# Kernel tuning notes

Measured on AMD Instinct MI355X. Metric: run time of the kernel, lower is better.

## Reference

```python
import jax, jax.numpy as jnp
import numpy as np

D_MODEL = 1024
NUM_HEADS = 16
BATCH = 2
SEQ = 2048


def setup_inputs() -> dict:
    key = jax.random.key(0)
    ks = jax.random.split(key, 5)
    scale = 1.0 / np.sqrt(D_MODEL)
    x = jax.random.normal(ks[0], (BATCH, SEQ, D_MODEL), dtype=jnp.float32)
    Wq = jax.random.normal(ks[1], (D_MODEL, D_MODEL), dtype=jnp.float32) * scale
    Wk = jax.random.normal(ks[2], (D_MODEL, D_MODEL), dtype=jnp.float32) * scale
    Wv = jax.random.normal(ks[3], (D_MODEL, D_MODEL), dtype=jnp.float32) * scale
    Wo = jax.random.normal(ks[4], (D_MODEL, D_MODEL), dtype=jnp.float32) * scale
    return {"x": x, "Wq": Wq, "Wk": Wk, "Wv": Wv, "Wo": Wo}


def reference(x, Wq, Wk, Wv, Wo):
    b, s, d_model = x.shape
    h = NUM_HEADS
    d_head = d_model // h
    # projections (Linear with weight [out,in]: y = x @ W^T)
    def split_heads(y):
        return y.reshape(b, s, h, d_head).transpose(0, 2, 1, 3)  # b h s d
    q = split_heads(x @ Wq.T)
    k = split_heads(x @ Wk.T)
    v = split_heads(x @ Wv.T)
    # full (non-flash) attention, as in the original
    att = jnp.einsum('bhsd,bhtd->bhst', q, k) / jnp.sqrt(jnp.float32(d_head)).astype(x.dtype)
    att = jax.nn.softmax(att, axis=-1)
    out = jnp.einsum('bhst,bhtd->bhsd', att, v)
    out = out.transpose(0, 2, 1, 3).reshape(b, s, d_model)
    return out @ Wo.T
```

## Files before the change

kernel.cpp:

```cpp
#include <hip/hip_runtime.h>
#include <stdint.h>

typedef __bf16 bf16_t;
typedef __bf16 bf16x4 __attribute__((ext_vector_type(4)));
typedef __bf16 bf16x8 __attribute__((ext_vector_type(8)));
typedef float  f32x4  __attribute__((ext_vector_type(4)));
typedef float  f32x16 __attribute__((ext_vector_type(16)));

#define D_MODEL 1024
#define SEQ     2048
#define BATCH   2
#define NHEAD   16
#define DHEAD   64
#define NROWS   (BATCH*SEQ)
#define LDT     72

#define QSCALE  (0.125f * 1.4426950408889634f)

__device__ __forceinline__ void async_ld16(const bf16_t* g, bf16_t* l) {
    __builtin_amdgcn_global_load_lds(
        (const __attribute__((address_space(1))) uint32_t*)(uintptr_t)g,
        (__attribute__((address_space(3))) uint32_t*)(uintptr_t)l,
        16, 0, 0);
}

__device__ __forceinline__ bf16x8 cvt8(f32x4 lo, f32x4 hi) {
    bf16x8 o;
#pragma unroll
    for (int i = 0; i < 4; ++i) { o[i] = (bf16_t)lo[i]; o[4 + i] = (bf16_t)hi[i]; }
    return o;
}

__device__ __forceinline__ void plswap(uint32_t& a, uint32_t& b) {
    asm("v_permlane32_swap_b32 %0, %1" : "+v"(a), "+v"(b));
}

__device__ __forceinline__ uint32_t cvtpk(float lo, float hi) {
    uint32_t r;
    asm("v_cvt_pk_bf16_f32 %0, %1, %2" : "=v"(r) : "v"(lo), "v"(hi));
    return r;
}

__global__ void __launch_bounds__(256)
k_cvt(const float* __restrict__ w0, const float* __restrict__ w1,
      const float* __restrict__ w2, const float* __restrict__ w3,
      const float* __restrict__ x,
      bf16_t* __restrict__ o0, bf16_t* __restrict__ o1,
      bf16_t* __restrict__ o2, bf16_t* __restrict__ o3,
      bf16_t* __restrict__ ox)
{
    const int blk = blockIdx.x;
    const float* s; bf16_t* d; int bi;
    if (blk < 2048) { s = x; d = ox; bi = blk; }
    else {
        const int t = blk - 2048, sel = t >> 9; bi = t & 511;
        s = (sel == 0) ? w0 : (sel == 1) ? w1 : (sel == 2) ? w2 : w3;
        d = (sel == 0) ? o0 : (sel == 1) ? o1 : (sel == 2) ? o2 : o3;
    }
    const size_t i = ((size_t)bi * 256 + threadIdx.x) * 8;
    *(bf16x8*)(d + i) = cvt8(*(const f32x4*)(s + i), *(const f32x4*)(s + i + 4));
}

template <int OUT_MODE, int MT>
__device__ __forceinline__ void gemmT(bf16_t* __restrict__ smem,
                                      const bf16_t* __restrict__ X,
                                      const bf16_t* __restrict__ W,
                                      void* __restrict__ Yv,
                                      int m0, int n0, float oscale)
{
    constexpr int FM = MT / 32;
    bf16_t* lA = smem;
    bf16_t* lB = smem + MT * 32;

    const int tid  = threadIdx.x;
    const int lane = tid & 63;
    const int w    = tid >> 6;
    const int l15  = lane & 15;
    const int quad = lane >> 4;

    const int cB0 = tid, cB1 = tid + 256;
    const int rB0 = cB0 >> 2, rB1 = cB1 >> 2;
    const int kB0 = (cB0 & 3) ^ ((rB0 >> 1) & 3);
    const int kB1 = (cB1 & 3) ^ ((rB1 >> 1) & 3);
    const bf16_t* gB0 = W + (size_t)(n0 + rB0) * D_MODEL + kB0 * 8;
    const bf16_t* gB1 = W + (size_t)(n0 + rB1) * D_MODEL + kB1 * 8;

    const int cA0 = tid;
    const int rA0 = cA0 >> 2;
    const int kA0 = (cA0 & 3) ^ ((rA0 >> 1) & 3);
    const bf16_t* gA0 = X + (size_t)(m0 + rA0) * D_MODEL + kA0 * 8;
    const int cA1 = tid + 256;
    const int rA1 = cA1 >> 2;
    const int kA1 = (cA1 & 3) ^ ((rA1 >> 1) & 3);
    const bf16_t* gA1 = X + (size_t)(m0 + rA1) * D_MODEL + kA1 * 8;

    int am[FM], bn[4];
    const int mw = (w >> 1) * (MT / 2), nw = (w & 1) * 64;
#pragma unroll
    for (int i = 0; i < FM; ++i) {
        const int ra = mw + i * 16 + l15;
        am[i] = ra * 32 + (quad ^ ((ra >> 1) & 3)) * 8;
    }
#pragma unroll
    for (int i = 0; i < 4; ++i) {
        const int rb = nw + i * 16 + l15;
        bn[i] = rb * 32 + (quad ^ ((rb >> 1) & 3)) * 8;
    }

    f32x4 acc[FM][4];
#pragma unroll
    for (int i = 0; i < FM; ++i)
#pragma unroll
        for (int j = 0; j < 4; ++j) acc[i][j] = f32x4{0.f, 0.f, 0.f, 0.f};

    for (int k0 = 0; k0 < D_MODEL; k0 += 32) {
        __syncthreads();
        async_ld16(gA0 + k0, &lA[cA0 * 8]);
        if constexpr (MT == 128) async_ld16(gA1 + k0, &lA[cA1 * 8]);
        async_ld16(gB0 + k0, &lB[cB0 * 8]);
        async_ld16(gB1 + k0, &lB[cB1 * 8]);
        __syncthreads();

        bf16x8 af[FM], bfr[4];
#pragma unroll
        for (int i = 0; i < FM; ++i) af[i] = *(const bf16x8*)&lA[am[i]];
#pragma unroll
        for (int i = 0; i < 4; ++i) bfr[i] = *(const bf16x8*)&lB[bn[i]];
#pragma unroll
        for (int mi = 0; mi < FM; ++mi)
#pragma unroll
            for (int ni = 0; ni < 4; ++ni)
                acc[mi][ni] = __builtin_amdgcn_mfma_f32_16x16x32_bf16(
                    af[mi], bfr[ni], acc[mi][ni], 0, 0, 0);
    }

    if constexpr (OUT_MODE == 1) {
        bf16_t* lT = smem;
#pragma unroll
        for (int h0 = 0; h0 < 2; ++h0) {
            __syncthreads();
            if ((w >> 1) == h0) {
#pragma unroll
                for (int mi = 0; mi < FM; ++mi)
#pragma unroll
                    for (int ni = 0; ni < 4; ++ni) {
                        bf16x4 pk;
#pragma unroll
                        for (int r = 0; r < 4; ++r)
                            pk[r] = (bf16_t)(acc[mi][ni][r] * oscale);
                        const int col = nw + ni * 16 + l15;
                        *(bf16x4*)&lT[col * LDT + mi * 16 + quad * 4] = pk;
                    }
            }
            __syncthreads();
            const int col = tid & 127;
            const int seg = tid >> 7;
            const int brow = m0 + h0 * 64;
            const int b = brow >> 11, sb = brow & 2047;
            const int cg = n0 + col;
            bf16_t* dst = (bf16_t*)Yv +
                ((size_t)((b << 4) | (cg >> 6)) * 64 + (cg & 63)) * SEQ + sb;
#pragma unroll
            for (int u = 0; u < 4; ++u)
                *(bf16x8*)(dst + seg * 32 + u * 8) =
                    *(const bf16x8*)&lT[col * LDT + seg * 32 + u * 8];
        }
    } else {
#pragma unroll
        for (int mi = 0; mi < FM; ++mi)
#pragma unroll
            for (int ni = 0; ni < 4; ++ni)
#pragma unroll
                for (int r = 0; r < 4; ++r) {
                    const int row = m0 + mw + mi * 16 + quad * 4 + r;
                    const int col = n0 + nw + ni * 16 + l15;
                    const float vv = acc[mi][ni][r] * oscale;
                    if constexpr (OUT_MODE == 0)
                        ((bf16_t*)Yv)[(size_t)row * D_MODEL + col] = (bf16_t)vv;
                    else
                        ((float*)Yv)[(size_t)row * D_MODEL + col] = vv;
                }
    }
}

__global__ void __launch_bounds__(256, 3)
k_gemm_qkv(const bf16_t* __restrict__ X,
           const bf16_t* __restrict__ Wq, const bf16_t* __restrict__ Wk,
           const bf16_t* __restrict__ Wv,
           bf16_t* __restrict__ Qb, bf16_t* __restrict__ Kb, bf16_t* __restrict__ Vt)
{
    __shared__ __align__(16) bf16_t smem[128 * LDT];
    const int id = blockIdx.x + 32 * blockIdx.y;
    const int s  = (id & 7) * 96 + (id >> 3);
    const int m0 = (s & 31) * 128;
    const int yp = s >> 5;
    const int sel = yp >> 3;
    const int n0  = (yp & 7) * 128;
    if (sel == 0)      gemmT<0,128>(smem, X, Wq, Qb, m0, n0, QSCALE);
    else if (sel == 1) gemmT<0,128>(smem, X, Wk, Kb, m0, n0, 1.0f);
    else               gemmT<1,128>(smem, X, Wv, Vt, m0, n0, 1.0f);
}

__global__ void __launch_bounds__(256, 2)
k_gemm_out(const bf16_t* __restrict__ X, const bf16_t* __restrict__ W,
           float* __restrict__ Y)
{
    __shared__ __align__(16) bf16_t smem[64 * 32 + 128 * 32];
    const int id = blockIdx.x + 64 * blockIdx.y;
    const int s  = (id & 7) * 64 + (id >> 3);
    const int m0 = (s & 63) * 64;
    const int n0 = (s >> 6) * 128;
    gemmT<2,64>(smem, X, W, Y, m0, n0, 1.0f);
}

__global__ void __launch_bounds__(256, 2)
k_attn(const bf16_t* __restrict__ Qb, const bf16_t* __restrict__ Kb,
       const bf16_t* __restrict__ Vt, bf16_t* __restrict__ Ob)
{
    __shared__ __align__(16) char arena[51200];
    bf16_t* lK = (bf16_t*)arena;
    bf16_t* lV = (bf16_t*)(arena + 24576);

    const int tid  = threadIdx.x;
    const int lane = tid & 63;
    const int w    = tid >> 6;
    const int wq   = w >> 1;
    const int wk   = w & 1;
    const int l31  = lane & 31;
    const int h    = lane >> 5;

    const int i_  = blockIdx.x + 32 * blockIdx.y;
    const int bh  = 4 * (i_ & 7) + ((i_ >> 3) & 3);
    const int q0  = (i_ >> 5) * 128;
    const int b_ = bh >> 4, hh = bh & 15;

    const size_t base = (size_t)b_ * SEQ * D_MODEL + (size_t)hh * DHEAD;
    const bf16_t* Qp = Qb + base;
    const bf16_t* Kp = Kb + base;
    const bf16_t* Vp = Vt + (size_t)bh * DHEAD * SEQ;

    bf16x8 qf[2][4];
#pragma unroll
    for (int qh = 0; qh < 2; ++qh) {
        const int qrow = q0 + wq * 64 + qh * 32 + l31;
#pragma unroll
        for (int c = 0; c < 4; ++c)
            qf[qh][c] = *(const bf16x8*)&Qp[(size_t)qrow * D_MODEL + c * 16 + h * 8];
    }

    const int c0 = tid, c1 = tid + 256;
    const int r0 = c0 >> 3, g0 = (c0 & 7) ^ (r0 & 7);
    const int r1 = r0 + 32;
    const bf16_t* gK0 = Kp + (size_t)r0 * D_MODEL + g0 * 8;
    const bf16_t* gK1 = Kp + (size_t)r1 * D_MODEL + g0 * 8;
    const bf16_t* gV0 = Vp + (size_t)r0 * SEQ + g0 * 8;
    const bf16_t* gV1 = Vp + (size_t)r1 * SEQ + g0 * 8;

    int koff[4], voff[2][2];
#pragma unroll
    for (int c = 0; c < 4; ++c) {
        const int row = wk * 32 + l31;
        koff[c] = row * 64 + (((2 * c + h) ^ (row & 7)) * 8);
    }
#pragma unroll
    for (int a = 0; a < 2; ++a)
#pragma unroll
        for (int ck = 0; ck < 2; ++ck) {
            const int row = a * 32 + l31;
            const int ch  = 4 * wk + 2 * ck + h;
            voff[a][ck] = row * 64 + ((ch ^ (row & 7)) * 8);
        }

    bf16x8 onef;
#pragma unroll
    for (int i = 0; i < 8; ++i) onef[i] = (bf16_t)1.0f;

    f32x16 fz;
#pragma unroll
    for (int i = 0; i < 16; ++i) fz[i] = 0.f;

    f32x16 acc_o[2][2];
    f32x16 acc_s[2];
#pragma unroll
    for (int qh = 0; qh < 2; ++qh) {
#pragma unroll
        for (int i = 0; i < 16; ++i) {
            acc_o[qh][0][i] = 0.f; acc_o[qh][1][i] = 0.f; acc_s[qh][i] = 0.f;
        }
    }

    auto STAGE = [&](int tile, int buf) {
        const size_t kv0 = (size_t)tile * 64;
        bf16_t* dK = lK + buf * 4096;
        bf16_t* dV = lV + buf * 4096;
        async_ld16(gK0 + kv0 * D_MODEL, &dK[c0 * 8]);
        async_ld16(gK1 + kv0 * D_MODEL, &dK[c1 * 8]);
        async_ld16(gV0 + kv0, &dV[c0 * 8]);
        async_ld16(gV1 + kv0, &dV[c1 * 8]);
    };

    STAGE(0, 0);
    STAGE(1, 1);
    asm volatile("s_waitcnt vmcnt(4)\n\ts_barrier" ::: "memory");

    int cb = 0;
    const int NT = SEQ / 64;
    for (int t = 0; t < NT; ++t) {
        if (t + 2 < NT) STAGE(t + 2, cb == 0 ? 2 : cb - 1);
        const bf16_t* lKc = lK + cb * 4096;
        const bf16_t* lVc = lV + cb * 4096;

        bf16x8 kf[4];
#pragma unroll
        for (int c = 0; c < 4; ++c) kf[c] = *(const bf16x8*)&lKc[koff[c]];

        f32x16 st[2];
        __builtin_amdgcn_s_setprio(1);
#pragma unroll
        for (int qh = 0; qh < 2; ++qh) {
            st[qh] = __builtin_amdgcn_mfma_f32_32x32x16_bf16(
                kf[0], qf[qh][0], fz, 0, 0, 0);
#pragma unroll
            for (int c = 1; c < 4; ++c)
                st[qh] = __builtin_amdgcn_mfma_f32_32x32x16_bf16(
                    kf[c], qf[qh][c], st[qh], 0, 0, 0);
        }
        __builtin_amdgcn_s_setprio(0);

        uint32_t pd[2][4][2];
#pragma unroll
        for (int qh = 0; qh < 2; ++qh)
#pragma unroll
            for (int g = 0; g < 4; ++g) {
                pd[qh][g][0] = cvtpk(__builtin_amdgcn_exp2f(st[qh][g * 4 + 0]),
                                     __builtin_amdgcn_exp2f(st[qh][g * 4 + 1]));
                pd[qh][g][1] = cvtpk(__builtin_amdgcn_exp2f(st[qh][g * 4 + 2]),
                                     __builtin_amdgcn_exp2f(st[qh][g * 4 + 3]));
            }

        bf16x8 pf[2][2];
#pragma unroll
        for (int qh = 0; qh < 2; ++qh)
#pragma unroll
            for (int ck = 0; ck < 2; ++ck) {
                uint32_t a0 = pd[qh][2 * ck][0],     b0 = pd[qh][2 * ck + 1][0];
                uint32_t a1 = pd[qh][2 * ck][1],     b1 = pd[qh][2 * ck + 1][1];
                plswap(a0, b0);
                plswap(a1, b1);
                union { bf16x8 v; uint32_t d[4]; } up;
                up.d[0] = a0; up.d[1] = a1; up.d[2] = b0; up.d[3] = b1;
                pf[qh][ck] = up.v;
            }

        __builtin_amdgcn_s_setprio(1);
#pragma unroll
        for (int qh = 0; qh < 2; ++qh)
#pragma unroll
            for (int ck = 0; ck < 2; ++ck)
                acc_s[qh] = __builtin_amdgcn_mfma_f32_32x32x16_bf16(
                    pf[qh][ck], onef, acc_s[qh], 0, 0, 0);
#pragma unroll
        for (int a = 0; a < 2; ++a)
#pragma unroll
            for (int ck = 0; ck < 2; ++ck) {
                bf16x8 vf = *(const bf16x8*)&lVc[voff[a][ck]];
#pragma unroll
                for (int qh = 0; qh < 2; ++qh)
                    acc_o[qh][a] = __builtin_amdgcn_mfma_f32_32x32x16_bf16(
                        pf[qh][ck], vf, acc_o[qh][a], 0, 0, 0);
            }
        __builtin_amdgcn_s_setprio(0);

        if (t + 2 < NT)
            asm volatile("s_waitcnt vmcnt(4) lgkmcnt(0)\n\ts_barrier" ::: "memory");
        else
            asm volatile("s_waitcnt vmcnt(0) lgkmcnt(0)\n\ts_barrier" ::: "memory");
        cb = (cb == 2) ? 0 : cb + 1;
    }

    union F16 { f32x16 v; f32x4 q[4]; };
    float* blob = (float*)arena + ((size_t)(wq * 64 + lane)) * 100;

    if (wk) {
#pragma unroll
        for (int qh = 0; qh < 2; ++qh) {
#pragma unroll
            for (int a = 0; a < 2; ++a) {
                F16 u; u.v = acc_o[qh][a];
#pragma unroll
                for (int i = 0; i < 4; ++i)
                    *(f32x4*)&blob[(qh * 8 + a * 4 + i) * 4] = u.q[i];
            }
            F16 s; s.v = acc_s[qh];
#pragma unroll
            for (int i = 0; i < 4; ++i)
                *(f32x4*)&blob[64 + (qh * 4 + i) * 4] = s.q[i];
        }
    }
    __syncthreads();
    if (!wk) {
#pragma unroll
        for (int qh = 0; qh < 2; ++qh) {
#pragma unroll
            for (int a = 0; a < 2; ++a) {
                F16 u; u.v = acc_o[qh][a];
#pragma unroll
                for (int i = 0; i < 4; ++i)
                    u.q[i] += *(const f32x4*)&blob[(qh * 8 + a * 4 + i) * 4];
                acc_o[qh][a] = u.v;
            }
            F16 s; s.v = acc_s[qh];
#pragma unroll
            for (int i = 0; i < 4; ++i)
                s.q[i] += *(const f32x4*)&blob[64 + (qh * 4 + i) * 4];
            acc_s[qh] = s.v;
        }

#pragma unroll
        for (int qh = 0; qh < 2; ++qh)
#pragma unroll
            for (int g = 0; g < 4; ++g)
#pragma unroll
                for (int r = 0; r < 4; ++r) {
                    const float inv = 1.0f / acc_s[qh][g * 4 + r];
                    const int row = b_ * SEQ + q0 + wq * 64 + qh * 32 + (r + 8 * g + 4 * h);
                    const size_t rb = (size_t)row * D_MODEL + hh * DHEAD + l31;
                    Ob[rb]      = (bf16_t)(acc_o[qh][0][g * 4 + r] * inv);
                    Ob[rb + 32] = (bf16_t)(acc_o[qh][1][g * 4 + r] * inv);
                }
    }
}

extern "C" void kernel_launch(void* const* d_in, const int* in_sizes, int n_in,
                              void* d_out, int out_size, void* d_ws, size_t ws_size,
                              hipStream_t stream)
{
    const float* x  = (const float*)d_in[0];
    const float* Wq = (const float*)d_in[1];
    const float* Wk = (const float*)d_in[2];
    const float* Wv = (const float*)d_in[3];
    const float* Wo = (const float*)d_in[4];
    float* out = (float*)d_out;

    const size_t wmat = (size_t)D_MODEL * D_MODEL;
    const size_t mat  = (size_t)NROWS * D_MODEL;
    bf16_t* Wqb = (bf16_t*)d_ws;
    bf16_t* Wkb = Wqb + wmat;
    bf16_t* Wvb = Wkb + wmat;
    bf16_t* Wob = Wvb + wmat;
    bf16_t* Xb  = Wob + wmat;
    bf16_t* Qb  = Xb + mat;
    bf16_t* Kb  = Qb + mat;
    bf16_t* Vt  = Kb + mat;
    bf16_t* Ab  = Qb;

    dim3 blk(256);
    k_cvt<<<dim3(4096), blk, 0, stream>>>(Wq, Wk, Wv, Wo, x, Wqb, Wkb, Wvb, Wob, Xb);
    k_gemm_qkv<<<dim3(32, 24), blk, 0, stream>>>(Xb, Wqb, Wkb, Wvb, Qb, Kb, Vt);
    k_attn<<<dim3(32, 16), blk, 0, stream>>>(Qb, Kb, Vt, Ab);
    k_gemm_out<<<dim3(64, 8), blk, 0, stream>>>(Ab, Wob, out);
}
```

Baseline: 183.7 us.

## Process two KV tiles per barrier with double-buffered 128-row stages

The attention loop now stages 128 keys/values per iteration into a 64KB double buffer instead of 64 keys into a triple buffer. This halves the number of barriers and waits per sequence and lets the two sub-tiles' QK MFMAs issue back to back. It also drops the inline cvt_pk asm in favour of compiler bf16 casts and removes the block-index swizzle. The larger LDS footprint may cut occupancy from two blocks per CU, and the wait now drains all loads (vmcnt(0)) each iteration, which reduces how far loads can run ahead.

```diff
diff --git a/kernel.cpp b/kernel.cpp
--- a/kernel.cpp
+++ b/kernel.cpp
@@ -33,12 +33,6 @@
 
 __device__ __forceinline__ void plswap(uint32_t& a, uint32_t& b) {
     asm("v_permlane32_swap_b32 %0, %1" : "+v"(a), "+v"(b));
-}
-
-__device__ __forceinline__ uint32_t cvtpk(float lo, float hi) {
-    uint32_t r;
-    asm("v_cvt_pk_bf16_f32 %0, %1, %2" : "=v"(r) : "v"(lo), "v"(hi));
-    return r;
 }
 
 __global__ void __launch_bounds__(256)
@@ -217,9 +211,8 @@
 k_attn(const bf16_t* __restrict__ Qb, const bf16_t* __restrict__ Kb,
        const bf16_t* __restrict__ Vt, bf16_t* __restrict__ Ob)
 {
-    __shared__ __align__(16) char arena[51200];
-    bf16_t* lK = (bf16_t*)arena;
-    bf16_t* lV = (bf16_t*)(arena + 24576);
+    __shared__ __align__(16) char arena[65536];
+    bf16_t* lKV = (bf16_t*)arena;
 
     const int tid  = threadIdx.x;
     const int lane = tid & 63;
@@ -229,10 +222,9 @@
     const int l31  = lane & 31;
     const int h    = lane >> 5;
 
-    const int i_  = blockIdx.x + 32 * blockIdx.y;
-    const int bh  = 4 * (i_ & 7) + ((i_ >> 3) & 3);
-    const int q0  = (i_ >> 5) * 128;
+    const int bh = blockIdx.x;
     const int b_ = bh >> 4, hh = bh & 15;
+    const int q0 = blockIdx.y * 128;
 
     const size_t base = (size_t)b_ * SEQ * D_MODEL + (size_t)hh * DHEAD;
     const bf16_t* Qp = Qb + base;
@@ -275,10 +267,6 @@
 #pragma unroll
     for (int i = 0; i < 8; ++i) onef[i] = (bf16_t)1.0f;
 
-    f32x16 fz;
-#pragma unroll
-    for (int i = 0; i < 16; ++i) fz[i] = 0.f;
-
     f32x16 acc_o[2][2];
     f32x16 acc_s[2];
 #pragma unroll
@@ -289,93 +277,141 @@
         }
     }
 
-    auto STAGE = [&](int tile, int buf) {
-        const size_t kv0 = (size_t)tile * 64;
-        bf16_t* dK = lK + buf * 4096;
-        bf16_t* dV = lV + buf * 4096;
-        async_ld16(gK0 + kv0 * D_MODEL, &dK[c0 * 8]);
-        async_ld16(gK1 + kv0 * D_MODEL, &dK[c1 * 8]);
-        async_ld16(gV0 + kv0, &dV[c0 * 8]);
-        async_ld16(gV1 + kv0, &dV[c1 * 8]);
+    auto STAGE = [&](int t, int buf) {
+        bf16_t* B = lKV + buf * 16384;
+#pragma unroll
+        for (int u = 0; u < 2; ++u) {
+            const size_t kv0 = (size_t)(t * 128 + u * 64);
+            async_ld16(gK0 + kv0 * D_MODEL, &B[u * 4096 + c0 * 8]);
+            async_ld16(gK1 + kv0 * D_MODEL, &B[u * 4096 + c1 * 8]);
+            async_ld16(gV0 + kv0, &B[8192 + u * 4096 + c0 * 8]);
+            async_ld16(gV1 + kv0, &B[8192 + u * 4096 + c1 * 8]);
+        }
     };
 
     STAGE(0, 0);
-    STAGE(1, 1);
-    asm volatile("s_waitcnt vmcnt(4)\n\ts_barrier" ::: "memory");
-
-    int cb = 0;
-    const int NT = SEQ / 64;
-    for (int t = 0; t < NT; ++t) {
-        if (t + 2 < NT) STAGE(t + 2, cb == 0 ? 2 : cb - 1);
-        const bf16_t* lKc = lK + cb * 4096;
-        const bf16_t* lVc = lV + cb * 4096;
-
-        bf16x8 kf[4];
-#pragma unroll
-        for (int c = 0; c < 4; ++c) kf[c] = *(const bf16x8*)&lKc[koff[c]];
-
-        f32x16 st[2];
+    asm volatile("s_waitcnt vmcnt(0)\n\ts_barrier" ::: "memory");
+
+    int cur = 0;
+    const int NT2 = SEQ / 128;
+    for (int t = 0; t < NT2; ++t) {
+        if (t + 1 < NT2) STAGE(t + 1, cur ^ 1);
+        const bf16_t* Bc = lKV + cur * 16384;
+        const bf16_t* lK0 = Bc;
+        const bf16_t* lK1 = Bc + 4096;
+        const bf16_t* lV0 = Bc + 8192;
+        const bf16_t* lV1 = Bc + 12288;
+
+        bf16x8 kf0[4], kf1[4];
+#pragma unroll
+        for (int c = 0; c < 4; ++c) kf0[c] = *(const bf16x8*)&lK0[koff[c]];
+#pragma unroll
+        for (int c = 0; c < 4; ++c) kf1[c] = *(const bf16x8*)&lK1[koff[c]];
+
+        f32x16 st0[2], st1[2];
+#pragma unroll
+        for (int qh = 0; qh < 2; ++qh)
+#pragma unroll
+            for (int i = 0; i < 16; ++i) { st0[qh][i] = 0.f; st1[qh][i] = 0.f; }
         __builtin_amdgcn_s_setprio(1);
 #pragma unroll
+        for (int qh = 0; qh < 2; ++qh)
+#pragma unroll
+            for (int c = 0; c < 4; ++c)
+                st0[qh] = __builtin_amdgcn_mfma_f32_32x32x16_bf16(
+                    kf0[c], qf[qh][c], st0[qh], 0, 0, 0);
+#pragma unroll
+        for (int qh = 0; qh < 2; ++qh)
+#pragma unroll
+            for (int c = 0; c < 4; ++c)
+                st1[qh] = __builtin_amdgcn_mfma_f32_32x32x16_bf16(
+                    kf1[c], qf[qh][c], st1[qh], 0, 0, 0);
+        __builtin_amdgcn_s_setprio(0);
+
+        bf16x8 pf0[2][2];
+#pragma unroll
         for (int qh = 0; qh < 2; ++qh) {
-            st[qh] = __builtin_amdgcn_mfma_f32_32x32x16_bf16(
-                kf[0], qf[qh][0], fz, 0, 0, 0);
-#pragma unroll
-            for (int c = 1; c < 4; ++c)
-                st[qh] = __builtin_amdgcn_mfma_f32_32x32x16_bf16(
-                    kf[c], qf[qh][c], st[qh], 0, 0, 0);
-        }
-        __builtin_amdgcn_s_setprio(0);
-
-        uint32_t pd[2][4][2];
-#pragma unroll
-        for (int qh = 0; qh < 2; ++qh)
-#pragma unroll
-            for (int g = 0; g < 4; ++g) {
-                pd[qh][g][0] = cvtpk(__builtin_amdgcn_exp2f(st[qh][g * 4 + 0]),
-                                     __builtin_amdgcn_exp2f(st[qh][g * 4 + 1]));
-                pd[qh][g][1] = cvtpk(__builtin_amdgcn_exp2f(st[qh][g * 4 + 2]),
-                                     __builtin_amdgcn_exp2f(st[qh][g * 4 + 3]));
-            }
-
-        bf16x8 pf[2][2];
-#pragma unroll
-        for (int qh = 0; qh < 2; ++qh)
+            bf16x4 pk[4];
+#pragma unroll
+            for (int g = 0; g < 4; ++g)
+#pragma unroll
+                for (int r = 0; r < 4; ++r)
+                    pk[g][r] = (bf16_t)__builtin_amdgcn_exp2f(st0[qh][g * 4 + r]);
 #pragma unroll
             for (int ck = 0; ck < 2; ++ck) {
-                uint32_t a0 = pd[qh][2 * ck][0],     b0 = pd[qh][2 * ck + 1][0];
-                uint32_t a1 = pd[qh][2 * ck][1],     b1 = pd[qh][2 * ck + 1][1];
+                union { bf16x4 v; uint32_t d[2]; } ua, ub;
+                ua.v = pk[2 * ck]; ub.v = pk[2 * ck + 1];
+                uint32_t a0 = ua.d[0], b0 = ub.d[0];
+                uint32_t a1 = ua.d[1], b1 = ub.d[1];
                 plswap(a0, b0);
                 plswap(a1, b1);
                 union { bf16x8 v; uint32_t d[4]; } up;
                 up.d[0] = a0; up.d[1] = a1; up.d[2] = b0; up.d[3] = b1;
-                pf[qh][ck] = up.v;
-            }
-
+                pf0[qh][ck] = up.v;
+            }
+        }
         __builtin_amdgcn_s_setprio(1);
 #pragma unroll
         for (int qh = 0; qh < 2; ++qh)
 #pragma unroll
             for (int ck = 0; ck < 2; ++ck)
                 acc_s[qh] = __builtin_amdgcn_mfma_f32_32x32x16_bf16(
-                    pf[qh][ck], onef, acc_s[qh], 0, 0, 0);
+                    pf0[qh][ck], onef, acc_s[qh], 0, 0, 0);
 #pragma unroll
         for (int a = 0; a < 2; ++a)
 #pragma unroll
             for (int ck = 0; ck < 2; ++ck) {
-                bf16x8 vf = *(const bf16x8*)&lVc[voff[a][ck]];
+                bf16x8 vf = *(const bf16x8*)&lV0[voff[a][ck]];
 #pragma unroll
                 for (int qh = 0; qh < 2; ++qh)
                     acc_o[qh][a] = __builtin_amdgcn_mfma_f32_32x32x16_bf16(
-                        pf[qh][ck], vf, acc_o[qh][a], 0, 0, 0);
+                        pf0[qh][ck], vf, acc_o[qh][a], 0, 0, 0);
             }
         __builtin_amdgcn_s_setprio(0);
 
-        if (t + 2 < NT)
-            asm volatile("s_waitcnt vmcnt(4) lgkmcnt(0)\n\ts_barrier" ::: "memory");
-        else
-            asm volatile("s_waitcnt vmcnt(0) lgkmcnt(0)\n\ts_barrier" ::: "memory");
-        cb = (cb == 2) ? 0 : cb + 1;
+        bf16x8 pf1[2][2];
+#pragma unroll
+        for (int qh = 0; qh < 2; ++qh) {
+            bf16x4 pk[4];
+#pragma unroll
+            for (int g = 0; g < 4; ++g)
+#pragma unroll
+                for (int r = 0; r < 4; ++r)
+                    pk[g][r] = (bf16_t)__builtin_amdgcn_exp2f(st1[qh][g * 4 + r]);
+#pragma unroll
+            for (int ck = 0; ck < 2; ++ck) {
+                union { bf16x4 v; uint32_t d[2]; } ua, ub;
+                ua.v = pk[2 * ck]; ub.v = pk[2 * ck + 1];
+                uint32_t a0 = ua.d[0], b0 = ub.d[0];
+                uint32_t a1 = ua.d[1], b1 = ub.d[1];
+                plswap(a0, b0);
+                plswap(a1, b1);
+                union { bf16x8 v; uint32_t d[4]; } up;
+                up.d[0] = a0; up.d[1] = a1; up.d[2] = b0; up.d[3] = b1;
+                pf1[qh][ck] = up.v;
+            }
+        }
+        __builtin_amdgcn_s_setprio(1);
+#pragma unroll
+        for (int qh = 0; qh < 2; ++qh)
+#pragma unroll
+            for (int ck = 0; ck < 2; ++ck)
+                acc_s[qh] = __builtin_amdgcn_mfma_f32_32x32x16_bf16(
+                    pf1[qh][ck], onef, acc_s[qh], 0, 0, 0);
+#pragma unroll
+        for (int a = 0; a < 2; ++a)
+#pragma unroll
+            for (int ck = 0; ck < 2; ++ck) {
+                bf16x8 vf = *(const bf16x8*)&lV1[voff[a][ck]];
+#pragma unroll
+                for (int qh = 0; qh < 2; ++qh)
+                    acc_o[qh][a] = __builtin_amdgcn_mfma_f32_32x32x16_bf16(
+                        pf1[qh][ck], vf, acc_o[qh][a], 0, 0, 0);
+            }
+        __builtin_amdgcn_s_setprio(0);
+
+        asm volatile("s_waitcnt vmcnt(0) lgkmcnt(0)\n\ts_barrier" ::: "memory");
+        cur ^= 1;
     }
 
     union F16 { f32x16 v; f32x4 q[4]; };
```

After: 183.0 us. Within noise of the previous version (-0.4%).

## Double-buffer QKV GEMM loads and simplify attention pipeline to two stages

Applied to the files above, without the earlier changes.

Adds a double-buffered LDS pipeline to the QKV projection GEMM so the next K-slice loads overlap with MFMA compute, which removes one barrier per iteration. The attention kernel moves from a three-stage to a two-stage K/V prefetch with a full vmcnt wait. It also drops the swizzled block-to-head mapping in favour of a direct grid mapping, and replaces the inline packed bf16 conversion with plain casts. The GEMM change trades extra LDS for overlap. The attention changes reduce latency hiding and cache locality, and may lower conversion efficiency.

```diff
diff --git a/kernel.cpp b/kernel.cpp
--- a/kernel.cpp
+++ b/kernel.cpp
@@ -35,12 +35,6 @@
     asm("v_permlane32_swap_b32 %0, %1" : "+v"(a), "+v"(b));
 }
 
-__device__ __forceinline__ uint32_t cvtpk(float lo, float hi) {
-    uint32_t r;
-    asm("v_cvt_pk_bf16_f32 %0, %1, %2" : "=v"(r) : "v"(lo), "v"(hi));
-    return r;
-}
-
 __global__ void __launch_bounds__(256)
 k_cvt(const float* __restrict__ w0, const float* __restrict__ w1,
       const float* __restrict__ w2, const float* __restrict__ w3,
@@ -61,16 +55,15 @@
     *(bf16x8*)(d + i) = cvt8(*(const f32x4*)(s + i), *(const f32x4*)(s + i + 4));
 }
 
-template <int OUT_MODE, int MT>
+template <int OUT_MODE, int MT, bool DBUF>
 __device__ __forceinline__ void gemmT(bf16_t* __restrict__ smem,
                                       const bf16_t* __restrict__ X,
                                       const bf16_t* __restrict__ W,
                                       void* __restrict__ Yv,
                                       int m0, int n0, float oscale)
 {
-    constexpr int FM = MT / 32;
-    bf16_t* lA = smem;
-    bf16_t* lB = smem + MT * 32;
+    constexpr int FM  = MT / 32;
+    constexpr int BUF = (MT + 128) * 32;
 
     const int tid  = threadIdx.x;
     const int lane = tid & 63;
@@ -113,14 +106,17 @@
 #pragma unroll
         for (int j = 0; j < 4; ++j) acc[i][j] = f32x4{0.f, 0.f, 0.f, 0.f};
 
-    for (int k0 = 0; k0 < D_MODEL; k0 += 32) {
-        __syncthreads();
+    auto STAGE = [&](int k0, int b) {
+        bf16_t* lA = smem + b * BUF;
+        bf16_t* lB = lA + MT * 32;
         async_ld16(gA0 + k0, &lA[cA0 * 8]);
         if constexpr (MT == 128) async_ld16(gA1 + k0, &lA[cA1 * 8]);
         async_ld16(gB0 + k0, &lB[cB0 * 8]);
         async_ld16(gB1 + k0, &lB[cB1 * 8]);
-        __syncthreads();
-
+    };
+    auto COMPUTE = [&](int b) {
+        const bf16_t* lA = smem + b * BUF;
+        const bf16_t* lB = lA + MT * 32;
         bf16x8 af[FM], bfr[4];
 #pragma unroll
         for (int i = 0; i < FM; ++i) af[i] = *(const bf16x8*)&lA[am[i]];
@@ -132,6 +128,25 @@
             for (int ni = 0; ni < 4; ++ni)
                 acc[mi][ni] = __builtin_amdgcn_mfma_f32_16x16x32_bf16(
                     af[mi], bfr[ni], acc[mi][ni], 0, 0, 0);
+    };
+
+    if constexpr (DBUF) {
+        STAGE(0, 0);
+        __syncthreads();
+        int buf = 0;
+        for (int k0 = 0; k0 < D_MODEL; k0 += 32) {
+            if (k0 + 32 < D_MODEL) STAGE(k0 + 32, buf ^ 1);
+            COMPUTE(buf);
+            __syncthreads();
+            buf ^= 1;
+        }
+    } else {
+        for (int k0 = 0; k0 < D_MODEL; k0 += 32) {
+            __syncthreads();
+            STAGE(k0, 0);
+            __syncthreads();
+            COMPUTE(0);
+        }
     }
 
     if constexpr (OUT_MODE == 1) {
@@ -189,16 +204,16 @@
            const bf16_t* __restrict__ Wv,
            bf16_t* __restrict__ Qb, bf16_t* __restrict__ Kb, bf16_t* __restrict__ Vt)
 {
-    __shared__ __align__(16) bf16_t smem[128 * LDT];
+    __shared__ __align__(16) bf16_t smem[16384];
     const int id = blockIdx.x + 32 * blockIdx.y;
     const int s  = (id & 7) * 96 + (id >> 3);
     const int m0 = (s & 31) * 128;
     const int yp = s >> 5;
     const int sel = yp >> 3;
     const int n0  = (yp & 7) * 128;
-    if (sel == 0)      gemmT<0,128>(smem, X, Wq, Qb, m0, n0, QSCALE);
-    else if (sel == 1) gemmT<0,128>(smem, X, Wk, Kb, m0, n0, 1.0f);
-    else               gemmT<1,128>(smem, X, Wv, Vt, m0, n0, 1.0f);
+    if (sel == 0)      gemmT<0,128,true>(smem, X, Wq, Qb, m0, n0, QSCALE);
+    else if (sel == 1) gemmT<0,128,true>(smem, X, Wk, Kb, m0, n0, 1.0f);
+    else               gemmT<1,128,true>(smem, X, Wv, Vt, m0, n0, 1.0f);
 }
 
 __global__ void __launch_bounds__(256, 2)
@@ -210,7 +225,7 @@
     const int s  = (id & 7) * 64 + (id >> 3);
     const int m0 = (s & 63) * 64;
     const int n0 = (s >> 6) * 128;
-    gemmT<2,64>(smem, X, W, Y, m0, n0, 1.0f);
+    gemmT<2,64,false>(smem, X, W, Y, m0, n0, 1.0f);
 }
 
 __global__ void __launch_bounds__(256, 2)
@@ -219,7 +234,7 @@
 {
     __shared__ __align__(16) char arena[51200];
     bf16_t* lK = (bf16_t*)arena;
-    bf16_t* lV = (bf16_t*)(arena + 24576);
+    bf16_t* lV = (bf16_t*)(arena + 16384);
 
     const int tid  = threadIdx.x;
     const int lane = tid & 63;
@@ -229,10 +244,9 @@
     const int l31  = lane & 31;
     const int h    = lane >> 5;
 
-    const int i_  = blockIdx.x + 32 * blockIdx.y;
-    const int bh  = 4 * (i_ & 7) + ((i_ >> 3) & 3);
-    const int q0  = (i_ >> 5) * 128;
+    const int bh = blockIdx.x;
     const int b_ = bh >> 4, hh = bh & 15;
+    const int q0 = blockIdx.y * 128;
 
     const size_t base = (size_t)b_ * SEQ * D_MODEL + (size_t)hh * DHEAD;
     const bf16_t* Qp = Qb + base;
@@ -275,10 +289,6 @@
 #pragma unroll
     for (int i = 0; i < 8; ++i) onef[i] = (bf16_t)1.0f;
 
-    f32x16 fz;
-#pragma unroll
-    for (int i = 0; i < 16; ++i) fz[i] = 0.f;
-
     f32x16 acc_o[2][2];
     f32x16 acc_s[2];
 #pragma unroll
@@ -289,62 +299,63 @@
         }
     }
 
-    auto STAGE = [&](int tile, int buf) {
-        const size_t kv0 = (size_t)tile * 64;
-        bf16_t* dK = lK + buf * 4096;
-        bf16_t* dV = lV + buf * 4096;
-        async_ld16(gK0 + kv0 * D_MODEL, &dK[c0 * 8]);
-        async_ld16(gK1 + kv0 * D_MODEL, &dK[c1 * 8]);
-        async_ld16(gV0 + kv0, &dV[c0 * 8]);
-        async_ld16(gV1 + kv0, &dV[c1 * 8]);
-    };
-
-    STAGE(0, 0);
-    STAGE(1, 1);
-    asm volatile("s_waitcnt vmcnt(4)\n\ts_barrier" ::: "memory");
-
-    int cb = 0;
+    async_ld16(gK0, &lK[c0 * 8]);
+    async_ld16(gK1, &lK[c1 * 8]);
+    async_ld16(gV0, &lV[c0 * 8]);
+    async_ld16(gV1, &lV[c1 * 8]);
+    asm volatile("s_waitcnt vmcnt(0)\n\ts_barrier" ::: "memory");
+
+    int cur = 0;
     const int NT = SEQ / 64;
     for (int t = 0; t < NT; ++t) {
-        if (t + 2 < NT) STAGE(t + 2, cb == 0 ? 2 : cb - 1);
-        const bf16_t* lKc = lK + cb * 4096;
-        const bf16_t* lVc = lV + cb * 4096;
+        if (t + 1 < NT) {
+            const int kv0 = (t + 1) * 64;
+            const int nb = (cur ^ 1) * 4096;
+            async_ld16(gK0 + (size_t)kv0 * D_MODEL, &lK[nb + c0 * 8]);
+            async_ld16(gK1 + (size_t)kv0 * D_MODEL, &lK[nb + c1 * 8]);
+            async_ld16(gV0 + kv0, &lV[nb + c0 * 8]);
+            async_ld16(gV1 + kv0, &lV[nb + c1 * 8]);
+        }
+        const bf16_t* lKc = lK + cur * 4096;
+        const bf16_t* lVc = lV + cur * 4096;
 
         bf16x8 kf[4];
 #pragma unroll
         for (int c = 0; c < 4; ++c) kf[c] = *(const bf16x8*)&lKc[koff[c]];
 
         f32x16 st[2];
+#pragma unroll
+        for (int qh = 0; qh < 2; ++qh)
+#pragma unroll
+            for (int i = 0; i < 16; ++i) st[qh][i] = 0.f;
         __builtin_amdgcn_s_setprio(1);
 #pragma unroll
-        for (int qh = 0; qh < 2; ++qh) {
-            st[qh] = __builtin_amdgcn_mfma_f32_32x32x16_bf16(
-                kf[0], qf[qh][0], fz, 0, 0, 0);
-#pragma unroll
-            for (int c = 1; c < 4; ++c)
+        for (int qh = 0; qh < 2; ++qh)
+#pragma unroll
+            for (int c = 0; c < 4; ++c)
                 st[qh] = __builtin_amdgcn_mfma_f32_32x32x16_bf16(
                     kf[c], qf[qh][c], st[qh], 0, 0, 0);
-        }
         __builtin_amdgcn_s_setprio(0);
 
-        uint32_t pd[2][4][2];
-#pragma unroll
-        for (int qh = 0; qh < 2; ++qh)
-#pragma unroll
-            for (int g = 0; g < 4; ++g) {
-                pd[qh][g][0] = cvtpk(__builtin_amdgcn_exp2f(st[qh][g * 4 + 0]),
-                                     __builtin_amdgcn_exp2f(st[qh][g * 4 + 1]));
-                pd[qh][g][1] = cvtpk(__builtin_amdgcn_exp2f(st[qh][g * 4 + 2]),
-                                     __builtin_amdgcn_exp2f(st[qh][g * 4 + 3]));
-            }
+        bf16x4 pk[2][4];
+#pragma unroll
+        for (int qh = 0; qh < 2; ++qh)
+#pragma unroll
+            for (int g = 0; g < 4; ++g)
+#pragma unroll
+                for (int r = 0; r < 4; ++r)
+                    pk[qh][g][r] = (bf16_t)__builtin_amdgcn_exp2f(st[qh][g * 4 + r]);
 
         bf16x8 pf[2][2];
 #pragma unroll
         for (int qh = 0; qh < 2; ++qh)
 #pragma unroll
             for (int ck = 0; ck < 2; ++ck) {
-                uint32_t a0 = pd[qh][2 * ck][0],     b0 = pd[qh][2 * ck + 1][0];
-                uint32_t a1 = pd[qh][2 * ck][1],     b1 = pd[qh][2 * ck + 1][1];
+                union { bf16x4 v; uint32_t d[2]; } ua, ub;
+                ua.v = pk[qh][2 * ck];
+                ub.v = pk[qh][2 * ck + 1];
+                uint32_t a0 = ua.d[0], b0 = ub.d[0];
+                uint32_t a1 = ua.d[1], b1 = ub.d[1];
                 plswap(a0, b0);
                 plswap(a1, b1);
                 union { bf16x8 v; uint32_t d[4]; } up;
@@ -371,11 +382,8 @@
             }
         __builtin_amdgcn_s_setprio(0);
 
-        if (t + 2 < NT)
-            asm volatile("s_waitcnt vmcnt(4) lgkmcnt(0)\n\ts_barrier" ::: "memory");
-        else
-            asm volatile("s_waitcnt vmcnt(0) lgkmcnt(0)\n\ts_barrier" ::: "memory");
-        cb = (cb == 2) ? 0 : cb + 1;
+        asm volatile("s_waitcnt vmcnt(0) lgkmcnt(0)\n\ts_barrier" ::: "memory");
+        cur ^= 1;
     }
 
     union F16 { f32x16 v; f32x4 q[4]; };
```

Result: faster. 179.1 us (-2.5%).
